# Kernel optimization log

Measured on AMD Instinct MI355X. Metric: run time of the kernel, lower is better.

Reference implementation:

```python
import jax, jax.numpy as jnp
import numpy as np

N_NODES = 50000
N_EDGES = 1600000
IN_FEATS = 128
ENC_H = 20
DEC_H = 64


def setup_inputs() -> dict:
    key = jax.random.key(0)
    ks = jax.random.split(key, 14)
    inp = {}
    inp["x"] = jax.random.normal(ks[0], (N_NODES, IN_FEATS), dtype=jnp.float32)
    inp["edge_index"] = jax.random.randint(ks[1], (2, N_EDGES), 0, N_NODES, dtype=jnp.int64)
    inp["node_id"] = 0
    inp["noise_normal"] = jax.random.normal(ks[2], (N_EDGES, ENC_H), dtype=jnp.float32)
    inp["noise_u"] = jax.random.uniform(ks[3], (N_EDGES, 1), dtype=jnp.float32)
    # parameters (glorot-ish init)
    def lin(k, fan_in, fan_out):
        s = 1.0 / np.sqrt(fan_in)
        return jax.random.uniform(k, (fan_in, fan_out), jnp.float32, -s, s)
    inp["W_gc"] = lin(ks[4], IN_FEATS, ENC_H)
    inp["b_gc"] = jnp.zeros((ENC_H,), jnp.float32)
    inp["W_mu"] = lin(ks[5], 3 * ENC_H, ENC_H)
    inp["b_mu"] = jnp.zeros((ENC_H,), jnp.float32)
    inp["W_var"] = lin(ks[6], 3 * ENC_H, ENC_H)
    inp["b_var"] = jnp.zeros((ENC_H,), jnp.float32)
    inp["W_d1"] = lin(ks[7], ENC_H, DEC_H)
    inp["b_d1"] = jnp.zeros((DEC_H,), jnp.float32)
    inp["W_d2"] = lin(ks[8], DEC_H, 1)
    inp["b_d2"] = jnp.zeros((1,), jnp.float32)
    return inp


def _gcn_conv(x, edge_index, W, b):
    """PyG-style GCNConv: add self-loops, symmetric D^-1/2 (A+I) D^-1/2 norm."""
    n = x.shape[0]
    sl = jnp.arange(n, dtype=edge_index.dtype)
    row = jnp.concatenate([edge_index[0], sl])  # source
    col = jnp.concatenate([edge_index[1], sl])  # target
    xw = x @ W  # [N, H]
    deg = jax.ops.segment_sum(jnp.ones_like(col, dtype=xw.dtype), col, num_segments=n)
    dinv = jnp.where(deg > 0, jax.lax.rsqrt(deg), 0.0)
    norm = dinv[row] * dinv[col]  # [E+N]
    out = jax.ops.segment_sum(xw[row] * norm[:, None], col, num_segments=n)
    return out + b


def reference(x, edge_index, node_id, noise_normal, noise_u,
              W_gc, b_gc, W_mu, b_mu, W_var, b_var, W_d1, b_d1, W_d2, b_d2):
    # GCN encoder
    x1 = jax.nn.relu(_gcn_conv(x, edge_index, W_gc, b_gc))  # [N, H]
    # per-edge concat: [src_embed | dst_embed | node_id_embed]
    rows, cols = edge_index[0], edge_index[1]
    node_embed = jnp.broadcast_to(x1[node_id][None, :], (rows.shape[0], x1.shape[1]))
    x2 = jnp.concatenate([x1[rows], x1[cols], node_embed], axis=1)  # [E, 3H]
    # variational heads + reparameterization
    mu = x2 @ W_mu + b_mu
    sigma = jnp.exp(x2 @ W_var + b_var)
    z = mu + sigma * noise_normal  # [E, H]
    # decoder MLP
    h = jax.nn.relu(z @ W_d1 + b_d1)
    sampling_weights = jax.nn.relu(h @ W_d2 + b_d2)  # [E, 1]
    # gumbel-sigmoid sample (training=True, bias=0.0 -> bias'=1e-4, temperature=1.0)
    bias = 0.0001
    eps = (bias - (1.0 - bias)) * noise_u + (1.0 - bias)
    gate = jnp.log(eps) - jnp.log(1.0 - eps) + sampling_weights
    return jax.nn.sigmoid(gate)
```

## Files before the change

### kernel.cpp

```cpp
#include <hip/hip_runtime.h>

#define NFEAT 128
#define H 20
#define DH 64
#define SCAN_T 1024
#define BE 64
#define CAP 128

typedef __attribute__((ext_vector_type(8))) short short8;
typedef __attribute__((ext_vector_type(4))) float f32x4;

__device__ __forceinline__ unsigned short f2bf(float f) {
    union { float f; unsigned u; } v; v.f = f;
    unsigned r = v.u + 0x7fff + ((v.u >> 16) & 1);
    return (unsigned short)(r >> 16);
}
__device__ __forceinline__ unsigned pk2(unsigned short a, unsigned short b) {
    return (unsigned)a | ((unsigned)b << 16);
}

template <int CTRL>
__device__ __forceinline__ float dpp_add(float x) {
    int y = __builtin_amdgcn_update_dpp(0, __float_as_int(x), CTRL, 0xF, 0xF, true);
    return x + __int_as_float(y);
}
__device__ __forceinline__ float sum16(float x) {
    x = dpp_add<0xB1>(x);
    x = dpp_add<0x4E>(x);
    x = dpp_add<0x124>(x);
    x = dpp_add<0x128>(x);
    return x;
}

__global__ __launch_bounds__(256) void k_prep(const float* __restrict__ Wmu, const float* __restrict__ Wvar,
                                              const float* __restrict__ Wd1,
                                              const float* __restrict__ bmu, const float* __restrict__ bvar,
                                              unsigned short* __restrict__ Bh, unsigned short* __restrict__ Bd1,
                                              float* __restrict__ bcat, int* __restrict__ deg, int N) {
    int t = blockIdx.x * blockDim.x + threadIdx.x;
    if (t < N) deg[t] = 0;
    if (t < 512) {
        int f = t >> 6, l = t & 63;
        int tile = f >> 1, s = f & 1;
        int col = (tile & 1) * 16 + (l & 15);
        const float* W = (tile < 2) ? Wmu : Wvar;
#pragma unroll
        for (int j = 0; j < 8; j++) {
            int k = s * 32 + (l >> 4) * 8 + j;
            float v = (k < 3 * H && col < H) ? W[k * H + col] : 0.f;
            Bh[(size_t)f * 512 + l * 8 + j] = f2bf(v);
        }
    } else if (t < 768) {
        int f = (t - 512) >> 6, l = t & 63;
        int n = f * 16 + (l & 15);
#pragma unroll
        for (int j = 0; j < 8; j++) {
            int k = (l >> 4) * 8 + j;
            float v = (k < H) ? Wd1[k * DH + n] : 0.f;
            Bd1[(size_t)f * 512 + l * 8 + j] = f2bf(v);
        }
    } else if (t < 808) {
        int c = t - 768;
        bcat[c] = (c < H) ? bmu[c] : bvar[c - H];
    }
}

__global__ __launch_bounds__(256) void k_bucket_slots(const int* __restrict__ rows, const int* __restrict__ cols,
                                                      int* __restrict__ deg, int* __restrict__ slots, int E) {
    int e = blockIdx.x * blockDim.x + threadIdx.x;
    if (e >= E) return;
    int c = cols[e];
    int pos = atomicAdd(&deg[c], 1);
    if (pos < CAP) slots[(size_t)c * CAP + pos] = rows[e];
}

__global__ __launch_bounds__(256) void k_deg(const int* __restrict__ cols, int* __restrict__ deg, int E) {
    int t = blockIdx.x * blockDim.x + threadIdx.x;
    if (t < E) atomicAdd(&deg[cols[t]], 1);
}

__global__ __launch_bounds__(SCAN_T) void k_scan(const int* __restrict__ deg, int* __restrict__ offsets,
                                                 int* __restrict__ cursor, int N) {
    __shared__ int sums[SCAN_T];
    int t = threadIdx.x;
    int chunk = (N + SCAN_T - 1) / SCAN_T;
    int beg = t * chunk;
    int end = min(beg + chunk, N);
    int s = 0;
    for (int i = beg; i < end; i++) s += deg[i];
    sums[t] = s;
    __syncthreads();
    for (int off = 1; off < SCAN_T; off <<= 1) {
        int v = (t >= off) ? sums[t - off] : 0;
        __syncthreads();
        sums[t] += v;
        __syncthreads();
    }
    int run = (t == 0) ? 0 : sums[t - 1];
    for (int i = beg; i < end; i++) {
        offsets[i] = run;
        cursor[i] = run;
        run += deg[i];
    }
    if (t == SCAN_T - 1) offsets[N] = sums[SCAN_T - 1];
}

__global__ __launch_bounds__(256) void k_bucket_csr(const int* __restrict__ rows, const int* __restrict__ cols,
                                                    int* __restrict__ cursor, int* __restrict__ srcs, int E) {
    int e = blockIdx.x * blockDim.x + threadIdx.x;
    if (e >= E) return;
    int pos = atomicAdd(&cursor[cols[e]], 1);
    srcs[pos] = rows[e];
}

__global__ __launch_bounds__(256) void k_xw_xs(const float* __restrict__ x, const float* __restrict__ Wgc,
                                               const int* __restrict__ deg,
                                               float* __restrict__ xs, int N) {
    __shared__ float Ws[NFEAT * H];
    for (int i = threadIdx.x; i < NFEAT * H; i += blockDim.x) Ws[i] = Wgc[i];
    __syncthreads();
    int n = blockIdx.x * blockDim.x + threadIdx.x;
    if (n >= N) return;
    float acc[H];
#pragma unroll
    for (int j = 0; j < H; j++) acc[j] = 0.f;
    const float4* x4 = (const float4*)(x + (size_t)n * NFEAT);
#pragma unroll 4
    for (int k4 = 0; k4 < NFEAT / 4; k4++) {
        float4 xv = x4[k4];
#pragma unroll
        for (int s = 0; s < 4; s++) {
            float xk = (s == 0) ? xv.x : (s == 1) ? xv.y : (s == 2) ? xv.z : xv.w;
            const float4* wrow = (const float4*)(Ws + (k4 * 4 + s) * H);
#pragma unroll
            for (int q = 0; q < 5; q++) {
                float4 w = wrow[q];
                acc[q * 4 + 0] += xk * w.x;
                acc[q * 4 + 1] += xk * w.y;
                acc[q * 4 + 2] += xk * w.z;
                acc[q * 4 + 3] += xk * w.w;
            }
        }
    }
    float di = rsqrtf((float)(deg[n] + 1));
    float4* o = (float4*)(xs + (size_t)n * H);
#pragma unroll
    for (int q = 0; q < 5; q++)
        o[q] = make_float4(acc[q * 4 + 0] * di, acc[q * 4 + 1] * di, acc[q * 4 + 2] * di, acc[q * 4 + 3] * di);
}

__device__ __forceinline__ void gather_core16(const float* __restrict__ xs, const int* __restrict__ idx,
                                              int beg, int end, int n, int sl, int degn,
                                              const float* __restrict__ bgc, unsigned short* __restrict__ x1b) {
    float acc[H];
    if (sl == 0) {
        const float4* self = (const float4*)(xs + (size_t)n * H);
#pragma unroll
        for (int q = 0; q < 5; q++) {
            float4 v = self[q];
            acc[q * 4 + 0] = v.x; acc[q * 4 + 1] = v.y; acc[q * 4 + 2] = v.z; acc[q * 4 + 3] = v.w;
        }
    } else {
#pragma unroll
        for (int j = 0; j < H; j++) acc[j] = 0.f;
    }
#pragma unroll 2
    for (int i = beg + sl; i < end; i += 16) {
        int r = idx[i];
        const float4* p = (const float4*)(xs + (size_t)r * H);
#pragma unroll
        for (int q = 0; q < 5; q++) {
            float4 v = p[q];
            acc[q * 4 + 0] += v.x; acc[q * 4 + 1] += v.y; acc[q * 4 + 2] += v.z; acc[q * 4 + 3] += v.w;
        }
    }
#pragma unroll
    for (int j = 0; j < H; j++) acc[j] = sum16(acc[j]);
    if (sl == 0) {
        float di = rsqrtf((float)(degn + 1));
        unsigned o[10];
#pragma unroll
        for (int j = 0; j < 10; j++) {
            float v0 = fmaxf(di * acc[2 * j] + bgc[2 * j], 0.f);
            float v1 = fmaxf(di * acc[2 * j + 1] + bgc[2 * j + 1], 0.f);
            o[j] = pk2(f2bf(v0), f2bf(v1));
        }
        unsigned* dst = (unsigned*)(x1b + (size_t)n * H);
        *(uint4*)dst = make_uint4(o[0], o[1], o[2], o[3]);
        *(uint4*)(dst + 4) = make_uint4(o[4], o[5], o[6], o[7]);
        *(uint2*)(dst + 8) = make_uint2(o[8], o[9]);
    }
}

__global__ __launch_bounds__(256) void k_gather_slots(const float* __restrict__ xs, const int* __restrict__ slots,
                                                      const int* __restrict__ deg, const float* __restrict__ bgc,
                                                      unsigned short* __restrict__ x1b, int N) {
    int wave = (blockIdx.x * 256 + threadIdx.x) >> 6;
    int lane = threadIdx.x & 63;
    int n = wave * 4 + (lane >> 4);
    if (n >= N) return;
    int dg = deg[n];
    int d = min(dg, CAP);
    gather_core16(xs, slots + (size_t)n * CAP, 0, d, n, lane & 15, dg, bgc, x1b);
}

__global__ __launch_bounds__(256) void k_gather_csr(const float* __restrict__ xs, const int* __restrict__ srcs,
                                                    const int* __restrict__ offsets, const int* __restrict__ deg,
                                                    const float* __restrict__ bgc,
                                                    unsigned short* __restrict__ x1b, int N) {
    int wave = (blockIdx.x * 256 + threadIdx.x) >> 6;
    int lane = threadIdx.x & 63;
    int n = wave * 4 + (lane >> 4);
    if (n >= N) return;
    gather_core16(xs, srcs, offsets[n], offsets[n + 1], n, lane & 15, deg[n], bgc, x1b);
}

__global__ __launch_bounds__(256) void k_mlp(
    const unsigned short* __restrict__ x1b, const int* __restrict__ rows, const int* __restrict__ cols,
    const int* __restrict__ node_id, const float* __restrict__ noise_n, const float* __restrict__ noise_u,
    const unsigned short* __restrict__ Bh, const unsigned short* __restrict__ Bd1g,
    const float* __restrict__ bcat, const float* __restrict__ b_d1,
    const float* __restrict__ W_d2, const float* __restrict__ b_d2,
    float* __restrict__ out, int E) {

    __shared__ __align__(16) unsigned short BhL[8 * 512];
    __shared__ __align__(16) unsigned short Bd1L[4 * 512];
    __shared__ __align__(16) unsigned short x2s[BE * 72];
    __shared__ __align__(16) unsigned short A2[BE * 44];
    __shared__ float bcatL[40];
    __shared__ float bd1L[DH];
    __shared__ float wd2L[DH];
    __shared__ float uL[BE];
    __shared__ float bd2s;

    int tid = threadIdx.x;
    int e0 = blockIdx.x * BE;
    int l = tid & 63, w = tid >> 6;
    int m = l & 15, quad = l >> 4;
    int erow0 = w * 16 + quad * 4;

    float nz0[4], nz1[4];
#pragma unroll
    for (int r4 = 0; r4 < 4; r4++) {
        int e = e0 + erow0 + r4;
        int ec = (e < E) ? e : 0;
        nz0[r4] = noise_n[(size_t)ec * H + m];
        nz1[r4] = (m < 4) ? noise_n[(size_t)ec * H + 16 + m] : 0.f;
    }

    {
        const uint4* s4 = (const uint4*)Bh;
        uint4* d4 = (uint4*)BhL;
        for (int i = tid; i < 512; i += 256) d4[i] = s4[i];
        s4 = (const uint4*)Bd1g;
        d4 = (uint4*)Bd1L;
        d4[tid] = s4[tid];
        if (tid < 40) bcatL[tid] = bcat[tid];
        if (tid < DH) {
            bd1L[tid] = b_d1[tid];
            wd2L[tid] = W_d2[tid];
            int e = e0 + tid;
            uL[tid] = noise_u[e < E ? e : 0];
        }
        if (tid == 0) bd2s = b_d2[0];
    }

    {
        int le = tid >> 2, p = tid & 3;
        int e = e0 + le; if (e >= E) e = E - 1;
        int r = rows[e], c = cols[e];
        int nid = node_id[0];
#pragma unroll
        for (int ii = 0; ii < 4; ii++) {
            int i = p + ii * 4;
            unsigned* dst = (unsigned*)((char*)x2s + le * 144 + i * 8);
            if (i < 15) {
                int node = (i < 5) ? r : (i < 10) ? c : nid;
                int cc = (i < 5) ? i : (i < 10) ? i - 5 : i - 10;
                uint2 v = *(const uint2*)((const char*)x1b + (size_t)node * 40 + cc * 8);
                dst[0] = v.x;
                dst[1] = v.y;
            } else {
                dst[0] = 0u; dst[1] = 0u;
            }
        }
    }
    __syncthreads();

    f32x4 accs[4];
    {
        const char* arow = (const char*)x2s + (w * 16 + m) * 144 + quad * 16;
        short8 a0 = *(const short8*)(arow);
        short8 a1 = *(const short8*)(arow + 64);
#pragma unroll
        for (int t4 = 0; t4 < 4; t4++) {
            f32x4 acc = {0.f, 0.f, 0.f, 0.f};
            short8 b0 = *(const short8*)((const char*)BhL + (t4 * 2 + 0) * 1024 + l * 16);
            short8 b1 = *(const short8*)((const char*)BhL + (t4 * 2 + 1) * 1024 + l * 16);
            acc = __builtin_amdgcn_mfma_f32_16x16x32_bf16(a0, b0, acc, 0, 0, 0);
            acc = __builtin_amdgcn_mfma_f32_16x16x32_bf16(a1, b1, acc, 0, 0, 0);
            accs[t4] = acc;
        }
    }

    {
        float bm0 = bcatL[m];
        float bv0 = bcatL[20 + m];
        float bm1 = (m < 4) ? bcatL[16 + m] : 0.f;
        float bv1 = (m < 4) ? bcatL[36 + m] : 0.f;
#pragma unroll
        for (int r4 = 0; r4 < 4; r4++) {
            float z0 = accs[0][r4] + bm0 + expf(accs[2][r4] + bv0) * nz0[r4];
            *(unsigned short*)((char*)A2 + (erow0 + r4) * 88 + m * 2) = f2bf(z0);
            unsigned short z1v = 0;
            if (m < 4) z1v = f2bf(accs[1][r4] + bm1 + expf(accs[3][r4] + bv1) * nz1[r4]);
            *(unsigned short*)((char*)A2 + (erow0 + r4) * 88 + (16 + m) * 2) = z1v;
        }
    }
    __syncthreads();

    {
        short8 a2 = *(const short8*)((const char*)A2 + (w * 16 + m) * 88 + quad * 16);
        float p0 = 0.f, p1 = 0.f, p2 = 0.f, p3 = 0.f;
#pragma unroll
        for (int t4 = 0; t4 < 4; t4++) {
            f32x4 acc = {0.f, 0.f, 0.f, 0.f};
            short8 bb = *(const short8*)((const char*)Bd1L + t4 * 1024 + l * 16);
            acc = __builtin_amdgcn_mfma_f32_16x16x32_bf16(a2, bb, acc, 0, 0, 0);
            int col = t4 * 16 + m;
            float bias = bd1L[col], wo = wd2L[col];
            p0 += fmaxf(acc[0] + bias, 0.f) * wo;
            p1 += fmaxf(acc[1] + bias, 0.f) * wo;
            p2 += fmaxf(acc[2] + bias, 0.f) * wo;
            p3 += fmaxf(acc[3] + bias, 0.f) * wo;
        }
        p0 = sum16(p0); p1 = sum16(p1); p2 = sum16(p2); p3 = sum16(p3);
        if (m < 4) {
            float swv = (m == 0) ? p0 : (m == 1) ? p1 : (m == 2) ? p2 : p3;
            int leo = w * 16 + quad * 4 + m;
            int e = e0 + leo;
            if (e < E) {
                float sw = fmaxf(swv + bd2s, 0.f);
                float u = uL[leo];
                float ev = 0.9999f - 0.9998f * u;
                float gate = logf(ev) - logf(1.f - ev) + sw;
                out[e] = 1.f / (1.f + expf(-gate));
            }
        }
    }
}

extern "C" void kernel_launch(void* const* d_in, const int* in_sizes, int n_in,
                              void* d_out, int out_size, void* d_ws, size_t ws_size,
                              hipStream_t stream) {
    const int N = in_sizes[0] / NFEAT;
    const int E = in_sizes[1] / 2;

    const float* x       = (const float*)d_in[0];
    const int*   ei      = (const int*)d_in[1];
    const int*   rows    = ei;
    const int*   cols    = ei + E;
    const int*   node_id = (const int*)d_in[2];
    const float* noise_n = (const float*)d_in[3];
    const float* noise_u = (const float*)d_in[4];
    const float* Wgc  = (const float*)d_in[5];
    const float* bgc  = (const float*)d_in[6];
    const float* Wmu  = (const float*)d_in[7];
    const float* bmu  = (const float*)d_in[8];
    const float* Wvar = (const float*)d_in[9];
    const float* bvar = (const float*)d_in[10];
    const float* Wd1  = (const float*)d_in[11];
    const float* bd1  = (const float*)d_in[12];
    const float* Wd2  = (const float*)d_in[13];
    const float* bd2  = (const float*)d_in[14];
    float* out = (float*)d_out;

    const int B = 256;
    int gN  = (N + B - 1) / B;
    int gG  = (N + 15) / 16;
    int gE  = (E + B - 1) / B;
    int gM  = (E + BE - 1) / BE;

    char* ws = (char*)d_ws;
    bool slot_path = (ws_size >= (size_t)(200000 + (size_t)N * CAP * 4 + 4000000 + 2000000 + 16384));

    if (slot_path) {
        int*   deg   = (int*)ws;
        int*   slots = (int*)(ws + 200000);
        float* xs    = (float*)(ws + 200000 + (size_t)N * CAP * 4);
        char*  p     = ws + 200000 + (size_t)N * CAP * 4 + 4000000;
        unsigned short* x1b = (unsigned short*)p;
        unsigned short* Bh  = (unsigned short*)(p + 2000000);
        unsigned short* Bd1 = (unsigned short*)(p + 2008192);
        float* bcat  = (float*)(p + 2012288);

        k_prep<<<gN, B, 0, stream>>>(Wmu, Wvar, Wd1, bmu, bvar, Bh, Bd1, bcat, deg, N);
        k_bucket_slots<<<gE, B, 0, stream>>>(rows, cols, deg, slots, E);
        k_xw_xs<<<gN, B, 0, stream>>>(x, Wgc, deg, xs, N);
        k_gather_slots<<<gG, B, 0, stream>>>(xs, slots, deg, bgc, x1b, N);
        k_mlp<<<gM, B, 0, stream>>>(x1b, rows, cols, node_id, noise_n, noise_u,
                                    Bh, Bd1, bcat, bd1, Wd2, bd2, out, E);
    } else {
        int*   deg     = (int*)ws;
        int*   offsets = (int*)(ws + 200000);
        int*   cursor  = (int*)(ws + 400016);
        int*   srcs    = (int*)(ws + 600016);
        float* xs      = (float*)(ws + 7000016);
        unsigned short* x1b = (unsigned short*)(ws + 11000016);
        unsigned short* Bh  = (unsigned short*)(ws + 13000016);
        unsigned short* Bd1 = (unsigned short*)(ws + 13008208);
        float* bcat    = (float*)(ws + 13012304);

        k_prep<<<gN, B, 0, stream>>>(Wmu, Wvar, Wd1, bmu, bvar, Bh, Bd1, bcat, deg, N);
        k_deg<<<gE, B, 0, stream>>>(cols, deg, E);
        k_scan<<<1, SCAN_T, 0, stream>>>(deg, offsets, cursor, N);
        k_bucket_csr<<<gE, B, 0, stream>>>(rows, cols, cursor, srcs, E);
        k_xw_xs<<<gN, B, 0, stream>>>(x, Wgc, deg, xs, N);
        k_gather_csr<<<gG, B, 0, stream>>>(xs, srcs, offsets, deg, bgc, x1b, N);
        k_mlp<<<gM, B, 0, stream>>>(x1b, rows, cols, node_id, noise_n, noise_u,
                                    Bh, Bd1, bcat, bd1, Wd2, bd2, out, E);
    }
}
```

Baseline: 471.5 us.

## Read MLP weights from global directly, add nontemporal hints, simplify gate math

The MLP kernel no longer stages its weight tiles, biases and uniform noise in LDS. Each wave now loads them straight from global memory, which cuts LDS usage and sets launch bounds for 8 blocks per CU so occupancy can rise. Edge index and slot loads and stores in the bucketing and gather kernels use nontemporal hints. The gumbel-sigmoid is rewritten algebraically as ev/(ev+(1-ev)exp(-sw)), removing two logs. In exchange, the weights are fetched repeatedly through cache rather than shared once per block.

```diff
diff --git a/kernel.cpp b/kernel.cpp
--- a/kernel.cpp
+++ b/kernel.cpp
@@ -69,9 +69,10 @@
                                                       int* __restrict__ deg, int* __restrict__ slots, int E) {
     int e = blockIdx.x * blockDim.x + threadIdx.x;
     if (e >= E) return;
-    int c = cols[e];
+    int c = __builtin_nontemporal_load(cols + e);
+    int r = __builtin_nontemporal_load(rows + e);
     int pos = atomicAdd(&deg[c], 1);
-    if (pos < CAP) slots[(size_t)c * CAP + pos] = rows[e];
+    if (pos < CAP) __builtin_nontemporal_store(r, &slots[(size_t)c * CAP + pos]);
 }
 
 __global__ __launch_bounds__(256) void k_deg(const int* __restrict__ cols, int* __restrict__ deg, int E) {
@@ -166,7 +167,7 @@
     }
 #pragma unroll 2
     for (int i = beg + sl; i < end; i += 16) {
-        int r = idx[i];
+        int r = __builtin_nontemporal_load(idx + i);
         const float4* p = (const float4*)(xs + (size_t)r * H);
 #pragma unroll
         for (int q = 0; q < 5; q++) {
@@ -215,7 +216,7 @@
     gather_core16(xs, srcs, offsets[n], offsets[n + 1], n, lane & 15, deg[n], bgc, x1b);
 }
 
-__global__ __launch_bounds__(256) void k_mlp(
+__global__ __launch_bounds__(256, 8) void k_mlp(
     const unsigned short* __restrict__ x1b, const int* __restrict__ rows, const int* __restrict__ cols,
     const int* __restrict__ node_id, const float* __restrict__ noise_n, const float* __restrict__ noise_u,
     const unsigned short* __restrict__ Bh, const unsigned short* __restrict__ Bd1g,
@@ -223,15 +224,8 @@
     const float* __restrict__ W_d2, const float* __restrict__ b_d2,
     float* __restrict__ out, int E) {
 
-    __shared__ __align__(16) unsigned short BhL[8 * 512];
-    __shared__ __align__(16) unsigned short Bd1L[4 * 512];
     __shared__ __align__(16) unsigned short x2s[BE * 72];
     __shared__ __align__(16) unsigned short A2[BE * 44];
-    __shared__ float bcatL[40];
-    __shared__ float bd1L[DH];
-    __shared__ float wd2L[DH];
-    __shared__ float uL[BE];
-    __shared__ float bd2s;
 
     int tid = threadIdx.x;
     int e0 = blockIdx.x * BE;
@@ -246,23 +240,6 @@
         int ec = (e < E) ? e : 0;
         nz0[r4] = noise_n[(size_t)ec * H + m];
         nz1[r4] = (m < 4) ? noise_n[(size_t)ec * H + 16 + m] : 0.f;
-    }
-
-    {
-        const uint4* s4 = (const uint4*)Bh;
-        uint4* d4 = (uint4*)BhL;
-        for (int i = tid; i < 512; i += 256) d4[i] = s4[i];
-        s4 = (const uint4*)Bd1g;
-        d4 = (uint4*)Bd1L;
-        d4[tid] = s4[tid];
-        if (tid < 40) bcatL[tid] = bcat[tid];
-        if (tid < DH) {
-            bd1L[tid] = b_d1[tid];
-            wd2L[tid] = W_d2[tid];
-            int e = e0 + tid;
-            uL[tid] = noise_u[e < E ? e : 0];
-        }
-        if (tid == 0) bd2s = b_d2[0];
     }
 
     {
@@ -295,8 +272,8 @@
 #pragma unroll
         for (int t4 = 0; t4 < 4; t4++) {
             f32x4 acc = {0.f, 0.f, 0.f, 0.f};
-            short8 b0 = *(const short8*)((const char*)BhL + (t4 * 2 + 0) * 1024 + l * 16);
-            short8 b1 = *(const short8*)((const char*)BhL + (t4 * 2 + 1) * 1024 + l * 16);
+            short8 b0 = *(const short8*)(Bh + (t4 * 2 + 0) * 512 + l * 8);
+            short8 b1 = *(const short8*)(Bh + (t4 * 2 + 1) * 512 + l * 8);
             acc = __builtin_amdgcn_mfma_f32_16x16x32_bf16(a0, b0, acc, 0, 0, 0);
             acc = __builtin_amdgcn_mfma_f32_16x16x32_bf16(a1, b1, acc, 0, 0, 0);
             accs[t4] = acc;
@@ -304,10 +281,10 @@
     }
 
     {
-        float bm0 = bcatL[m];
-        float bv0 = bcatL[20 + m];
-        float bm1 = (m < 4) ? bcatL[16 + m] : 0.f;
-        float bv1 = (m < 4) ? bcatL[36 + m] : 0.f;
+        float bm0 = bcat[m];
+        float bv0 = bcat[20 + m];
+        float bm1 = (m < 4) ? bcat[16 + m] : 0.f;
+        float bv1 = (m < 4) ? bcat[36 + m] : 0.f;
 #pragma unroll
         for (int r4 = 0; r4 < 4; r4++) {
             float z0 = accs[0][r4] + bm0 + expf(accs[2][r4] + bv0) * nz0[r4];
@@ -325,10 +302,10 @@
 #pragma unroll
         for (int t4 = 0; t4 < 4; t4++) {
             f32x4 acc = {0.f, 0.f, 0.f, 0.f};
-            short8 bb = *(const short8*)((const char*)Bd1L + t4 * 1024 + l * 16);
+            short8 bb = *(const short8*)(Bd1g + t4 * 512 + l * 8);
             acc = __builtin_amdgcn_mfma_f32_16x16x32_bf16(a2, bb, acc, 0, 0, 0);
             int col = t4 * 16 + m;
-            float bias = bd1L[col], wo = wd2L[col];
+            float bias = b_d1[col], wo = W_d2[col];
             p0 += fmaxf(acc[0] + bias, 0.f) * wo;
             p1 += fmaxf(acc[1] + bias, 0.f) * wo;
             p2 += fmaxf(acc[2] + bias, 0.f) * wo;
@@ -340,11 +317,11 @@
             int leo = w * 16 + quad * 4 + m;
             int e = e0 + leo;
             if (e < E) {
-                float sw = fmaxf(swv + bd2s, 0.f);
-                float u = uL[leo];
+                float sw = fmaxf(swv + b_d2[0], 0.f);
+                float u = noise_u[e];
                 float ev = 0.9999f - 0.9998f * u;
-                float gate = logf(ev) - logf(1.f - ev) + sw;
-                out[e] = 1.f / (1.f + expf(-gate));
+                float t = expf(-sw);
+                out[e] = ev / (ev + (1.f - ev) * t);
             }
         }
     }
```

Result: no change. 469.2 us (-0.5%).
